# Kernel tuning notes

Measured on AMD Instinct MI355X. Metric: run time of the kernel, lower is better.

## Reference

```python
import jax, jax.numpy as jnp
import numpy as np

EMBED_DIM = 512
NUM_HEADS = 8
HEAD_DIM = EMBED_DIM // NUM_HEADS
SCALE = HEAD_DIM ** -0.5


def setup_inputs() -> dict:
    key = jax.random.key(0)
    ks = jax.random.split(key, 5)
    B, N, C = 4, 2048, EMBED_DIM
    s = 0.02
    return {
        "x": jax.random.normal(ks[0], (B, N, C), jnp.float32),
        "qkv_w": jax.random.normal(ks[1], (3 * C, C), jnp.float32) * s,
        "qkv_b": jax.random.normal(ks[2], (3 * C,), jnp.float32) * s,
        "proj_w": jax.random.normal(ks[3], (C, C), jnp.float32) * s,
        "proj_b": jax.random.normal(ks[4], (C,), jnp.float32) * s,
    }


def reference(x, qkv_w, qkv_b, proj_w, proj_b):
    B, N, C = x.shape
    H, D = NUM_HEADS, HEAD_DIM
    # qkv: (B, N, 3C) -> (3, B, H, N, D)
    qkv = x @ qkv_w.T + qkv_b
    qkv = qkv.reshape(B, N, 3, H, D).transpose(2, 0, 3, 1, 4)
    q, k, v = qkv[0], qkv[1], qkv[2]
    attn = jnp.einsum("bhnd,bhmd->bhnm", q, k) * SCALE  # (B,H,N,N)
    attn = jax.nn.softmax(attn, axis=-1)
    out = jnp.einsum("bhnm,bhmd->bhnd", attn, v)  # (B,H,N,D)
    out = out.transpose(0, 2, 1, 3).reshape(B, N, C)
    return out @ proj_w.T + proj_b
```

## Files before the change

kernel.cpp:

```cpp
#include <hip/hip_runtime.h>

#define ED 512
#define NH 8
#define HD 64
#define BB 4
#define SEQ 2048
#define MTOT (BB*SEQ)

typedef float f32x4 __attribute__((ext_vector_type(4)));
typedef float f32x16 __attribute__((ext_vector_type(16)));
typedef __bf16 bf16x8 __attribute__((ext_vector_type(8)));
typedef int i32x2 __attribute__((ext_vector_type(2)));
typedef unsigned int u32x4 __attribute__((ext_vector_type(4)));

__device__ __forceinline__ unsigned short f2bf(float f) {
  unsigned int u = __float_as_uint(f);
  u += 0x7FFFu + ((u >> 16) & 1u);
  return (unsigned short)(u >> 16);
}

__device__ __forceinline__ unsigned int cvtpk(float lo, float hi) {
  unsigned int r;
  asm volatile("v_cvt_pk_bf16_f32 %0, %1, %2" : "=v"(r) : "v"(lo), "v"(hi));
  return r;
}

__device__ __forceinline__ void async16(const void* g, void* l) {
  auto gp = (const __attribute__((address_space(1))) unsigned int*)(uintptr_t)(g);
  auto lp = (__attribute__((address_space(3))) unsigned int*)(uintptr_t)(l);
  __builtin_amdgcn_global_load_lds(gp, lp, 16, 0, 0);
}

#define N4_X   1048576
#define N4_WQ  196608
#define N4_WP  65536
__global__ void cvt_all(const float* __restrict__ x,
                        const float* __restrict__ wq_in,
                        const float* __restrict__ wp_in,
                        unsigned short* __restrict__ xb,
                        unsigned short* __restrict__ wq,
                        unsigned short* __restrict__ wp) {
  int i = blockIdx.x * blockDim.x + threadIdx.x;
  const float* src; unsigned short* dst; int off;
  if (i < N4_X)              { src = x;     dst = xb; off = i; }
  else if (i < N4_X + N4_WQ) { src = wq_in; dst = wq; off = i - N4_X; }
  else                       { src = wp_in; dst = wp; off = i - (N4_X + N4_WQ); }
  float4 v = reinterpret_cast<const float4*>(src)[off];
  ushort4 o;
  o.x = f2bf(v.x); o.y = f2bf(v.y); o.z = f2bf(v.z); o.w = f2bf(v.w);
  reinterpret_cast<ushort4*>(dst)[off] = o;
}

template<int MODE, int BM>
__global__ __launch_bounds__(256)
void gemm_bt(const unsigned short* __restrict__ A,
             const unsigned short* __restrict__ B,
             const float* __restrict__ bias,
             int M, int N, int K,
             unsigned short* __restrict__ Qo,
             unsigned short* __restrict__ Ko,
             unsigned short* __restrict__ Vo,
             float* __restrict__ Co) {
  __shared__ __align__(16) unsigned short As[BM * 64];
  __shared__ __align__(16) unsigned short Bs[128 * 64];
  const int FI = BM / 32;
  const int t = threadIdx.x;
  const int l = t & 63;
  const int w = t >> 6;
  const int lo = l & 15, hi = l >> 4;
  const int wr = w >> 1, wc = w & 1;
  const int m0 = blockIdx.y * BM;
  const int n0 = blockIdx.x * 128;

  f32x4 acc[FI][4] = {};

  const int nkt = K >> 6;
  for (int kt = 0; kt < nkt; ++kt) {
    #pragma unroll
    for (int it = 0; it < BM / 32; ++it) {
      int c = it * 256 + t;
      int row = c >> 3, cin = c & 7;
      async16(A + (size_t)(m0 + row) * K + kt * 64 + cin * 8, &As[c * 8]);
    }
    #pragma unroll
    for (int it = 0; it < 4; ++it) {
      int c = it * 256 + t;
      int row = c >> 3, cin = c & 7;
      async16(B + (size_t)(n0 + row) * K + kt * 64 + cin * 8, &Bs[c * 8]);
    }
    asm volatile("s_waitcnt vmcnt(0)" ::: "memory");
    __syncthreads();
    #pragma unroll
    for (int kk = 0; kk < 2; ++kk) {
      bf16x8 af[FI], bf[4];
      #pragma unroll
      for (int i = 0; i < FI; ++i)
        af[i] = *reinterpret_cast<const bf16x8*>(
            &As[(wr * (BM / 2) + i * 16 + lo) * 64 + kk * 32 + hi * 8]);
      #pragma unroll
      for (int j = 0; j < 4; ++j)
        bf[j] = *reinterpret_cast<const bf16x8*>(
            &Bs[(wc * 64 + j * 16 + lo) * 64 + kk * 32 + hi * 8]);
      #pragma unroll
      for (int i = 0; i < FI; ++i)
        #pragma unroll
        for (int j = 0; j < 4; ++j)
          acc[i][j] = __builtin_amdgcn_mfma_f32_16x16x32_bf16(af[i], bf[j], acc[i][j], 0, 0, 0);
    }
    __syncthreads();
  }

  if (MODE == 0) {
    #pragma unroll
    for (int j = 0; j < 4; ++j) {
      int gcol = n0 + wc * 64 + j * 16 + lo;
      float bv = bias[gcol];
      int which = gcol >> 9;
      int h = (gcol >> 6) & 7;
      int d = gcol & 63;
      #pragma unroll
      for (int i = 0; i < FI; ++i) {
        int rbase = m0 + wr * (BM / 2) + i * 16 + hi * 4;
        int b = rbase >> 11;
        size_t bh = (size_t)(b * NH + h);
        if (which == 2) {
          ushort4 pk;
          pk.x = f2bf(acc[i][j][0] + bv);
          pk.y = f2bf(acc[i][j][1] + bv);
          pk.z = f2bf(acc[i][j][2] + bv);
          pk.w = f2bf(acc[i][j][3] + bv);
          int seq = rbase & 2047;
          *reinterpret_cast<ushort4*>(&Vo[(bh * HD + d) * SEQ + seq]) = pk;
        } else {
          #pragma unroll
          for (int e = 0; e < 4; ++e) {
            int seq = (rbase + e) & 2047;
            float v = acc[i][j][e] + bv;
            if (which == 0)
              Qo[(bh * SEQ + seq) * HD + d] = f2bf(v * 0.18033688f);
            else
              Ko[(bh * SEQ + seq) * HD + d] = f2bf(v);
          }
        }
      }
    }
  } else {
    #pragma unroll
    for (int j = 0; j < 4; ++j) {
      int gcol = n0 + wc * 64 + j * 16 + lo;
      float bv = bias[gcol];
      #pragma unroll
      for (int i = 0; i < FI; ++i) {
        int rbase = m0 + wr * (BM / 2) + i * 16 + hi * 4;
        #pragma unroll
        for (int e = 0; e < 4; ++e)
          Co[(size_t)(rbase + e) * N + gcol] = acc[i][j][e] + bv;
      }
    }
  }
}

__global__ __launch_bounds__(512, 4)
void attn_kernel(const unsigned short* __restrict__ Q,
                 const unsigned short* __restrict__ Kk,
                 const unsigned short* __restrict__ Vt,
                 unsigned short* __restrict__ Ao) {
  __shared__ __align__(16) unsigned short Ks[2][2][64 * 64];
  __shared__ __align__(16) unsigned short Vs[2][2][64 * 64];
  const int t = threadIdx.x;
  const int l = t & 63;
  const int wid = t >> 6;
  const int qg = wid & 3;
  const int kvh = wid >> 2;
  const int l31 = l & 31, lh = l >> 5;
  const int bh = blockIdx.y;
  const int q0 = blockIdx.x * 128;
  const int b = bh >> 3, h = bh & 7;

  bf16x8 qf[4];
  #pragma unroll
  for (int ks = 0; ks < 4; ++ks)
    qf[ks] = *reinterpret_cast<const bf16x8*>(
        &Q[((size_t)bh * SEQ + q0 + qg * 32 + l31) * HD + ks * 16 + lh * 8]);

  f32x16 o0 = {}, o1 = {}, osum = {};
  const __bf16 one1 = (__bf16)1.0f;
  const bf16x8 ones = {one1, one1, one1, one1, one1, one1, one1, one1};

  auto stage = [&](int buf, int kt) {
    const int half = t >> 8;
    const int tt = t & 255;
    const int sbase = half * 1024 + kt * 64;
    #pragma unroll
    for (int it = 0; it < 2; ++it) {
      int c = it * 256 + tt;
      int row = c >> 3, cin = c & 7;
      int sw = cin ^ (row & 7);
      async16(&Kk[((size_t)bh * SEQ + sbase + row) * HD + sw * 8],
              &Ks[half][buf][c * 8]);
    }
    #pragma unroll
    for (int it = 0; it < 2; ++it) {
      int c = it * 256 + tt;
      int row = c >> 3, cin = c & 7;
      int sw = cin ^ (row & 7);
      async16(&Vt[((size_t)bh * HD + row) * SEQ + sbase + sw * 8],
              &Vs[half][buf][c * 8]);
    }
  };

  auto tile = [&](int cur, int kt) {
    if (kt + 1 < 16) stage(cur ^ 1, kt + 1);

    #pragma unroll
    for (int kn = 0; kn < 2; ++kn) {
      f32x16 s = {};
      __builtin_amdgcn_s_setprio(1);
      #pragma unroll
      for (int ks = 0; ks < 4; ++ks) {
        int row = kn * 32 + l31;
        int ch = ((ks * 2 + lh) ^ (l31 & 7)) * 8;
        bf16x8 kf = *reinterpret_cast<const bf16x8*>(&Ks[kvh][cur][row * 64 + ch]);
        s = __builtin_amdgcn_mfma_f32_32x32x16_bf16(kf, qf[ks], s, 0, 0, 0);
      }
      __builtin_amdgcn_s_setprio(0);

      #pragma unroll
      for (int i = 0; i < 16; ++i) s[i] = __builtin_amdgcn_exp2f(s[i]);

      #pragma unroll
      for (int hs = 0; hs < 2; ++hs) {
        unsigned int w0 = cvtpk(s[8 * hs + 0], s[8 * hs + 1]);
        unsigned int w1 = cvtpk(s[8 * hs + 2], s[8 * hs + 3]);
        unsigned int w2 = cvtpk(s[8 * hs + 4], s[8 * hs + 5]);
        unsigned int w3 = cvtpk(s[8 * hs + 6], s[8 * hs + 7]);
        i32x2 r0 = __builtin_amdgcn_permlane32_swap((int)w0, (int)w2, false, false);
        i32x2 r1 = __builtin_amdgcn_permlane32_swap((int)w1, (int)w3, false, false);
        u32x4 fw = {(unsigned int)r0.x, (unsigned int)r1.x,
                    (unsigned int)r0.y, (unsigned int)r1.y};
        bf16x8 pf = __builtin_bit_cast(bf16x8, fw);

        int ss = kn * 2 + hs;
        int vch = ((ss * 2 + lh) ^ (l31 & 7)) * 8;
        __builtin_amdgcn_s_setprio(1);
        osum = __builtin_amdgcn_mfma_f32_32x32x16_bf16(pf, ones, osum, 0, 0, 0);
        bf16x8 vf0 = *reinterpret_cast<const bf16x8*>(&Vs[kvh][cur][l31 * 64 + vch]);
        bf16x8 vf1 = *reinterpret_cast<const bf16x8*>(&Vs[kvh][cur][(32 + l31) * 64 + vch]);
        o0 = __builtin_amdgcn_mfma_f32_32x32x16_bf16(pf, vf0, o0, 0, 0, 0);
        o1 = __builtin_amdgcn_mfma_f32_32x32x16_bf16(pf, vf1, o1, 0, 0, 0);
        __builtin_amdgcn_s_setprio(0);
      }
    }

    asm volatile("s_waitcnt vmcnt(0)" ::: "memory");
    __syncthreads();
  };

  stage(0, 0);
  asm volatile("s_waitcnt vmcnt(0)" ::: "memory");
  __syncthreads();

  for (int k2 = 0; k2 < 8; ++k2) {
    tile(0, 2 * k2);
    tile(1, 2 * k2 + 1);
  }

  float* lds = reinterpret_cast<float*>(&Ks[0][0][0]);
  if (kvh == 1) {
    int base = (qg * 64 + l) * 48;
    *reinterpret_cast<f32x16*>(&lds[base])      = o0;
    *reinterpret_cast<f32x16*>(&lds[base + 16]) = o1;
    *reinterpret_cast<f32x16*>(&lds[base + 32]) = osum;
  }
  __syncthreads();
  if (kvh == 0) {
    int base = (qg * 64 + l) * 48;
    o0   += *reinterpret_cast<const f32x16*>(&lds[base]);
    o1   += *reinterpret_cast<const f32x16*>(&lds[base + 16]);
    osum += *reinterpret_cast<const f32x16*>(&lds[base + 32]);

    #pragma unroll
    for (int r = 0; r < 16; ++r) {
      int qoff = (r & 3) + 8 * (r >> 2) + 4 * lh;
      int seq = q0 + qg * 32 + qoff;
      float inv = 1.f / osum[r];
      size_t base2 = ((size_t)b * SEQ + seq) * ED + h * HD;
      Ao[base2 + l31]      = f2bf(o0[r] * inv);
      Ao[base2 + 32 + l31] = f2bf(o1[r] * inv);
    }
  }
}

extern "C" void kernel_launch(void* const* d_in, const int* in_sizes, int n_in,
                              void* d_out, int out_size, void* d_ws, size_t ws_size,
                              hipStream_t stream) {
  const float* x      = (const float*)d_in[0];
  const float* qkv_w  = (const float*)d_in[1];
  const float* qkv_b  = (const float*)d_in[2];
  const float* proj_w = (const float*)d_in[3];
  const float* proj_b = (const float*)d_in[4];
  float* out = (float*)d_out;

  char* ws = (char*)d_ws;
  unsigned short* xb = (unsigned short*)(ws);
  unsigned short* wq = (unsigned short*)(ws + 8388608);
  unsigned short* wp = (unsigned short*)(ws + 9961472);
  unsigned short* Q  = (unsigned short*)(ws + 10485760);
  unsigned short* Kb = (unsigned short*)(ws + 18874368);
  unsigned short* Vt = (unsigned short*)(ws + 27262976);
  unsigned short* Ao = (unsigned short*)(ws + 35651584);

  cvt_all<<<(N4_X + N4_WQ + N4_WP + 255) / 256, 256, 0, stream>>>(
      x, qkv_w, proj_w, xb, wq, wp);

  dim3 g1(12, 64);
  gemm_bt<0, 128><<<g1, 256, 0, stream>>>(xb, wq, qkv_b, MTOT, 3 * ED, ED, Q, Kb, Vt, nullptr);

  dim3 ga(SEQ / 128, BB * NH);
  attn_kernel<<<ga, 512, 0, stream>>>(Q, Kb, Vt, Ao);

  dim3 g2(4, 128);
  gemm_bt<1, 64><<<g2, 256, 0, stream>>>(Ao, wp, proj_b, MTOT, ED, ED, nullptr, nullptr, nullptr, out);
}
```

Baseline: 97.81 us.

## Double-buffer GEMM LDS tiles with XOR swizzle and smaller QKV tile

Restructures the bf16 GEMM main loop so the next K-tile is fetched asynchronously into a second LDS buffer while MFMAs run on the current one. Adds an XOR swizzle on 16-byte chunks to reduce LDS bank conflicts on fragment reads, and raises wave priority around the MFMA block. Also switches the QKV projection to BM=64 tiles with twice as many blocks, aiming to fill more CUs. Doubling LDS per block may limit occupancy, and the smaller tile lowers data reuse per block.

Result: faster. 86.88 us (-11.2%).

```diff
diff --git a/kernel.cpp b/kernel.cpp
--- a/kernel.cpp
+++ b/kernel.cpp
@@ -61,8 +61,8 @@
              unsigned short* __restrict__ Ko,
              unsigned short* __restrict__ Vo,
              float* __restrict__ Co) {
-  __shared__ __align__(16) unsigned short As[BM * 64];
-  __shared__ __align__(16) unsigned short Bs[128 * 64];
+  __shared__ __align__(16) unsigned short As[2][BM * 64];
+  __shared__ __align__(16) unsigned short Bs[2][128 * 64];
   const int FI = BM / 32;
   const int t = threadIdx.x;
   const int l = t & 63;
@@ -74,39 +74,57 @@
 
   f32x4 acc[FI][4] = {};
 
-  const int nkt = K >> 6;
-  for (int kt = 0; kt < nkt; ++kt) {
+  auto stage = [&](int buf, int kt) {
     #pragma unroll
     for (int it = 0; it < BM / 32; ++it) {
       int c = it * 256 + t;
       int row = c >> 3, cin = c & 7;
-      async16(A + (size_t)(m0 + row) * K + kt * 64 + cin * 8, &As[c * 8]);
+      int sw = cin ^ (row & 7);
+      async16(A + (size_t)(m0 + row) * K + kt * 64 + sw * 8, &As[buf][c * 8]);
     }
     #pragma unroll
     for (int it = 0; it < 4; ++it) {
       int c = it * 256 + t;
       int row = c >> 3, cin = c & 7;
-      async16(B + (size_t)(n0 + row) * K + kt * 64 + cin * 8, &Bs[c * 8]);
-    }
-    asm volatile("s_waitcnt vmcnt(0)" ::: "memory");
-    __syncthreads();
+      int sw = cin ^ (row & 7);
+      async16(B + (size_t)(n0 + row) * K + kt * 64 + sw * 8, &Bs[buf][c * 8]);
+    }
+  };
+
+  const int nkt = K >> 6;
+  stage(0, 0);
+  asm volatile("s_waitcnt vmcnt(0)" ::: "memory");
+  __syncthreads();
+
+  for (int kt = 0; kt < nkt; ++kt) {
+    const int cur = kt & 1;
+    if (kt + 1 < nkt) stage(cur ^ 1, kt + 1);
+
+    __builtin_amdgcn_s_setprio(1);
     #pragma unroll
     for (int kk = 0; kk < 2; ++kk) {
       bf16x8 af[FI], bf[4];
       #pragma unroll
-      for (int i = 0; i < FI; ++i)
-        af[i] = *reinterpret_cast<const bf16x8*>(
-            &As[(wr * (BM / 2) + i * 16 + lo) * 64 + kk * 32 + hi * 8]);
-      #pragma unroll
-      for (int j = 0; j < 4; ++j)
-        bf[j] = *reinterpret_cast<const bf16x8*>(
-            &Bs[(wc * 64 + j * 16 + lo) * 64 + kk * 32 + hi * 8]);
+      for (int i = 0; i < FI; ++i) {
+        int ra = wr * (BM / 2) + i * 16 + lo;
+        int ch = (kk * 4 + hi) ^ (lo & 7);
+        af[i] = *reinterpret_cast<const bf16x8*>(&As[cur][ra * 64 + ch * 8]);
+      }
+      #pragma unroll
+      for (int j = 0; j < 4; ++j) {
+        int rb = wc * 64 + j * 16 + lo;
+        int ch = (kk * 4 + hi) ^ (lo & 7);
+        bf[j] = *reinterpret_cast<const bf16x8*>(&Bs[cur][rb * 64 + ch * 8]);
+      }
       #pragma unroll
       for (int i = 0; i < FI; ++i)
         #pragma unroll
         for (int j = 0; j < 4; ++j)
           acc[i][j] = __builtin_amdgcn_mfma_f32_16x16x32_bf16(af[i], bf[j], acc[i][j], 0, 0, 0);
     }
+    __builtin_amdgcn_s_setprio(0);
+
+    asm volatile("s_waitcnt vmcnt(0)" ::: "memory");
     __syncthreads();
   }
 
@@ -313,8 +331,8 @@
   cvt_all<<<(N4_X + N4_WQ + N4_WP + 255) / 256, 256, 0, stream>>>(
       x, qkv_w, proj_w, xb, wq, wp);
 
-  dim3 g1(12, 64);
-  gemm_bt<0, 128><<<g1, 256, 0, stream>>>(xb, wq, qkv_b, MTOT, 3 * ED, ED, Q, Kb, Vt, nullptr);
+  dim3 g1(12, 128);
+  gemm_bt<0, 64><<<g1, 256, 0, stream>>>(xb, wq, qkv_b, MTOT, 3 * ED, ED, Q, Kb, Vt, nullptr);
 
   dim3 ga(SEQ / 128, BB * NH);
   attn_kernel<<<ga, 512, 0, stream>>>(Q, Kb, Vt, Ao);
```
